# Kernel tuning notes

Measured on AMD Instinct MI355X. Metric: run time of the kernel, lower is better.

## Reference

```python
import jax, jax.numpy as jnp
import numpy as np

DET_SIZE = 5120
DET_THRESHOLD = 0.5
NMS_THRESHOLD = 0.4
STRIDES = (8, 16, 32)
NUM_ANCHORS = 2
TOP_K = 2048  # fixed pre-NMS candidate count (jit-friendly stand-in for torch.where filtering)


def _anchor_centers(stride):
    n = DET_SIZE // stride
    g = jnp.arange(n, dtype=jnp.float32) * stride
    X, Y = jnp.meshgrid(g, g, indexing='xy')       # matches torch.meshgrid(..., indexing='xy')
    c = jnp.stack([X, Y], axis=-1).reshape(-1, 2)  # (n*n, 2), x fastest
    return jnp.repeat(c, NUM_ANCHORS, axis=0)      # stack([c]*2, dim=1).reshape(-1,2) == interleaved repeat


def _pairwise_iou(b):
    # b: (K,4) xyxy
    area = jnp.clip(b[:, 2] - b[:, 0], 0.0) * jnp.clip(b[:, 3] - b[:, 1], 0.0)
    lt = jnp.maximum(b[:, None, :2], b[None, :, :2])
    rb = jnp.minimum(b[:, None, 2:], b[None, :, 2:])
    wh = jnp.clip(rb - lt, 0.0)
    inter = wh[..., 0] * wh[..., 1]
    return inter / (area[:, None] + area[None, :] - inter + 1e-9)


def _forward(scores8, bbox8, lms8, scores16, bbox16, lms16, scores32, bbox32, lms32, det_scale):
    confs, boxes, lmss = [], [], []
    per_stride = [(scores8, bbox8, lms8), (scores16, bbox16, lms16), (scores32, bbox32, lms32)]
    for (conf, bbox, lms), stride in zip(per_stride, STRIDES):
        c = _anchor_centers(stride)                 # (N,2)
        b = bbox * stride                            # distance-style offsets scaled by stride
        l = lms * stride
        box = jnp.concatenate([c - b[:, :2], c + b[:, 2:4]], axis=-1) / det_scale  # (N,4) xyxy
        pts = (c[:, None, :] + l.reshape(-1, 5, 2)) / det_scale                    # (N,5,2)
        confs.append(conf.reshape(-1)); boxes.append(box); lmss.append(pts)
    conf = jnp.concatenate(confs)
    box = jnp.concatenate(boxes, axis=0)
    pts = jnp.concatenate(lmss, axis=0)
    # score threshold via masking (fixed shapes); below-threshold entries get conf=-1
    conf_m = jnp.where(conf >= DET_THRESHOLD, conf, -1.0)
    top_conf, top_idx = jax.lax.top_k(conf_m, TOP_K)
    top_box = box[top_idx]          # (K,4)
    top_pts = pts[top_idx]          # (K,5,2)
    valid = top_conf >= DET_THRESHOLD
    iou = _pairwise_iou(top_box)    # (K,K)
    later = jnp.arange(TOP_K)
    def body(i, keep):
        supp = (iou[i] > NMS_THRESHOLD) & (later > i) & keep[i] & valid[i]
        return keep & ~supp
    keep = jax.lax.fori_loop(0, TOP_K, body, valid)  # greedy NMS in descending-score order
    m = keep.astype(top_box.dtype)
    # (K, 15) = [conf | bbox(4) | lms(10)], suppressed/invalid rows zeroed
    return jnp.concatenate([(top_conf * m)[:, None], top_box * m[:, None], top_pts.reshape(TOP_K, 10) * m[:, None]], axis=-1)


def setup_inputs() -> dict:
    key = jax.random.key(0)
    ks = jax.random.split(key, 9)
    inp = {}
    for i, s in enumerate(STRIDES):
        n = DET_SIZE // s
        N = n * n * NUM_ANCHORS
        inp[f'scores{s}'] = jax.random.uniform(ks[3 * i], (N,), dtype=jnp.float32)
        inp[f'bbox{s}'] = jax.random.uniform(ks[3 * i + 1], (N, 4), dtype=jnp.float32) * 8.0
        inp[f'lms{s}'] = jax.random.normal(ks[3 * i + 2], (N, 10), dtype=jnp.float32) * 4.0
    inp['det_scale'] = jnp.array(0.5, dtype=jnp.float32)
    return inp


def reference(scores8, bbox8, lms8, scores16, bbox16, lms16, scores32, bbox32, lms32, det_scale):
    return _forward(scores8, bbox8, lms8, scores16, bbox16, lms16, scores32, bbox32, lms32, det_scale)
```

## Files before the change

kernel.cpp:

```cpp
#include <hip/hip_runtime.h>
#include <stdint.h>
#include <stddef.h>

#pragma clang fp contract(off)

#define N8   819200u
#define N16  204800u
#define N32  51200u
#define NTOT 1075200u
#define TOPK 2048
#define CAND_MAX 8192
#define NBIN 8192u
#define BINSHIFT 10
#define NMS_THR 0.4f
#define DET_THR 0.5f

#define OFF_HIST   0u
#define OFF_META   32768u
#define OFF_CAND   32832u
#define OFF_TIDX   98368u
#define OFF_TCONF  106560u
#define OFF_BOX    114752u
#define OFF_DIAGT  147520u
#define OFF_SUPPT  155968u

__device__ __forceinline__ float load_conf(unsigned a, const float* __restrict__ s8,
                                           const float* __restrict__ s16,
                                           const float* __restrict__ s32) {
  if (a < N8) return s8[a];
  if (a < N8 + N16) return s16[a - N8];
  return s32[a - (N8 + N16)];
}

__device__ __forceinline__ void decode(unsigned a,
    const float* __restrict__ b8, const float* __restrict__ l8,
    const float* __restrict__ b16, const float* __restrict__ l16,
    const float* __restrict__ b32, const float* __restrict__ l32,
    float& cx, float& cy, float& s, const float*& bb, const float*& lm) {
  if (a < N8) {
    unsigned cell = a >> 1;
    cx = (float)((cell % 640u) * 8u); cy = (float)((cell / 640u) * 8u);
    s = 8.f; bb = b8 + (size_t)a * 4; lm = l8 + (size_t)a * 10;
  } else if (a < N8 + N16) {
    unsigned loc = a - N8; unsigned cell = loc >> 1;
    cx = (float)((cell % 320u) * 16u); cy = (float)((cell / 320u) * 16u);
    s = 16.f; bb = b16 + (size_t)loc * 4; lm = l16 + (size_t)loc * 10;
  } else {
    unsigned loc = a - (N8 + N16); unsigned cell = loc >> 1;
    cx = (float)((cell % 160u) * 32u); cy = (float)((cell / 160u) * 32u);
    s = 32.f; bb = b32 + (size_t)loc * 4; lm = l32 + (size_t)loc * 10;
  }
}

__global__ void k_hist(const float* __restrict__ s8, const float* __restrict__ s16,
                       const float* __restrict__ s32, unsigned* __restrict__ hist) {
  unsigned i = blockIdx.x * blockDim.x + threadIdx.x;
  unsigned st = gridDim.x * blockDim.x;
  for (unsigned a = i; a < NTOT; a += st) {
    float c = load_conf(a, s8, s16, s32);
    if (c >= DET_THR) {
      unsigned v = (__float_as_uint(c) - 0x3F000000u) >> BINSHIFT;
      if (v > NBIN - 1u) v = NBIN - 1u;
      atomicAdd(&hist[v], 1u);
    }
  }
}

__global__ void __launch_bounds__(1024) k_scan(const unsigned* __restrict__ hist,
                                               unsigned* __restrict__ meta) {
  __shared__ unsigned suf[1024];
  int t = threadIdx.x;
  const unsigned* hp = hist + (size_t)t * 8;
  unsigned s = 0;
  for (int b = 0; b < 8; b++) s += hp[b];
  suf[t] = s;
  __syncthreads();
  for (int d = 1; d < 1024; d <<= 1) {
    unsigned v = (t + d < 1024) ? suf[t + d] : 0u;
    __syncthreads();
    suf[t] += v;
    __syncthreads();
  }
  unsigned total = suf[0];
  unsigned mine = suf[t];
  unsigned nxt = (t < 1023) ? suf[t + 1] : 0u;
  if (total < (unsigned)TOPK) {
    if (t == 0) { meta[0] = 0u; meta[2] = total; }
    return;
  }
  if (mine >= (unsigned)TOPK && nxt < (unsigned)TOPK) {
    unsigned run = nxt, cut = (unsigned)t * 8u;
    for (int b = 7; b >= 0; b--) {
      run += hp[b];
      if (run >= (unsigned)TOPK) { cut = (unsigned)t * 8u + (unsigned)b; break; }
    }
    meta[0] = cut; meta[2] = total;
  }
}

__global__ void k_compact(const float* __restrict__ s8, const float* __restrict__ s16,
                          const float* __restrict__ s32, unsigned* __restrict__ meta,
                          unsigned long long* __restrict__ cand) {
  unsigned cut = meta[0];
  unsigned i = blockIdx.x * blockDim.x + threadIdx.x;
  unsigned st = gridDim.x * blockDim.x;
  for (unsigned a = i; a < NTOT; a += st) {
    float c = load_conf(a, s8, s16, s32);
    if (c >= DET_THR) {
      unsigned b = __float_as_uint(c);
      unsigned v = (b - 0x3F000000u) >> BINSHIFT;
      if (v >= cut) {
        unsigned pos = atomicAdd(&meta[3], 1u);
        if (pos < (unsigned)CAND_MAX)
          cand[pos] = ((unsigned long long)b << 32) |
                      (unsigned long long)(0xFFFFFFFFu - a);
      }
    }
  }
}

__global__ void __launch_bounds__(256) k_rank(
    const unsigned long long* __restrict__ cand, const unsigned* __restrict__ meta,
    const float* __restrict__ b8, const float* __restrict__ l8,
    const float* __restrict__ b16, const float* __restrict__ l16,
    const float* __restrict__ b32, const float* __restrict__ l32,
    const float* __restrict__ dsp,
    unsigned* __restrict__ tidx, float* __restrict__ tconf, float* __restrict__ box) {
  unsigned count = meta[3];
  if (count > (unsigned)CAND_MAX) count = (unsigned)CAND_MAX;
  unsigned wave = blockIdx.x * 4u + (threadIdx.x >> 6);
  unsigned lane = threadIdx.x & 63u;
  if (wave >= count) return;
  unsigned long long my = cand[wave];
  unsigned cnt = 0;
  for (unsigned i = lane; i < count; i += 64u)
    cnt += (cand[i] > my) ? 1u : 0u;
  for (int d = 32; d > 0; d >>= 1) cnt += __shfl_down(cnt, d);
  if (lane == 0 && cnt < (unsigned)TOPK) {
    unsigned r = cnt;
    unsigned a = 0xFFFFFFFFu - (unsigned)(my & 0xFFFFFFFFull);
    float conf = __uint_as_float((unsigned)(my >> 32));
    float cx, cy, s; const float* bb; const float* lm;
    decode(a, b8, l8, b16, l16, b32, l32, cx, cy, s, bb, lm);
    float ds = dsp[0];
    float b0 = bb[0] * s, b1 = bb[1] * s, b2 = bb[2] * s, b3 = bb[3] * s;
    box[r * 4 + 0] = (cx - b0) / ds;
    box[r * 4 + 1] = (cy - b1) / ds;
    box[r * 4 + 2] = (cx + b2) / ds;
    box[r * 4 + 3] = (cy + b3) / ds;
    tidx[r] = a; tconf[r] = conf;
  }
}

__global__ void __launch_bounds__(256) k_supp(const float* __restrict__ box,
                                              unsigned long long* __restrict__ supp64,
                                              unsigned* __restrict__ diagT) {
  int i = blockIdx.x;
  const float4 bi = ((const float4*)box)[i];
  float ai = fmaxf(bi.z - bi.x, 0.f) * fmaxf(bi.w - bi.y, 0.f);
  int tid = threadIdx.x;
  int lane = tid & 63, wv = tid >> 6;
  int c = i >> 5, k = i & 31;
  for (int base = 0; base < TOPK; base += 256) {
    int j = base + tid;
    const float4 bj = ((const float4*)box)[j];
    float aj = fmaxf(bj.z - bj.x, 0.f) * fmaxf(bj.w - bj.y, 0.f);
    float ltx = fmaxf(bi.x, bj.x), lty = fmaxf(bi.y, bj.y);
    float rbx = fminf(bi.z, bj.z), rby = fminf(bi.w, bj.w);
    float w = fmaxf(rbx - ltx, 0.f), h = fmaxf(rby - lty, 0.f);
    float inter = w * h;
    float iou = inter / (ai + aj - inter + 1e-9f);
    bool pred = (iou > NMS_THR) && (j > i);
    unsigned long long word = __ballot(pred);
    int w64 = (base >> 6) + wv;
    if (lane == 0) {
      supp64[(size_t)c * 1024 + k * 32 + w64] = word;
      if (w64 == (i >> 6))
        diagT[k * 64 + c] = (unsigned)(word >> (((i >> 5) & 1) * 32));
    }
  }
}

__global__ void __launch_bounds__(512) k_nms_out(
    const unsigned* __restrict__ supp_t, const unsigned* __restrict__ diagT,
    const unsigned* __restrict__ meta,
    const unsigned* __restrict__ tidx, const float* __restrict__ tconf,
    const float* __restrict__ b8, const float* __restrict__ l8,
    const float* __restrict__ b16, const float* __restrict__ l16,
    const float* __restrict__ b32, const float* __restrict__ l32,
    const float* __restrict__ dsp, float* __restrict__ out) {
  __shared__ unsigned keepw[64];
  __shared__ unsigned wacc[8];
  int tid = threadIdx.x;
  int v = tid >> 6, l = tid & 63;
  unsigned count = meta[3];
  if (count > (unsigned)TOPK) count = (unsigned)TOPK;
  if (tid < 8) wacc[tid] = 0u;
  unsigned dg[32];
  if (v == 0) {
#pragma unroll
    for (int k = 0; k < 32; k++) dg[k] = diagT[k * 64 + l];
  }
  int r = v * 4 + (l >> 4);
  int g = l & 15;
  const uint4* bp = (const uint4*)supp_t + ((size_t)r * 16 + g);
  uint4 P0 = bp[0 * 512], P1 = bp[1 * 512], P2 = bp[2 * 512], P3 = bp[3 * 512];
  uint4 A; A.x = 0u; A.y = 0u; A.z = 0u; A.w = 0u;
  __syncthreads();

#define STEP(PP, CC)                                                          \
  {                                                                           \
    const int ch = (CC);                                                      \
    if (v == 0) {                                                             \
      unsigned app = (l < 8) ? wacc[l] : 0u;                                  \
      app |= __shfl_xor(app, 1);                                              \
      app |= __shfl_xor(app, 2);                                              \
      app |= __shfl_xor(app, 4);                                              \
      unsigned appl = __builtin_amdgcn_readlane(app, 0);                      \
      unsigned lo = (unsigned)ch * 32u;                                       \
      unsigned init = (count >= lo + 32u) ? 0xFFFFFFFFu                       \
                    : (count <= lo ? 0u : ((1u << (count - lo)) - 1u));       \
      unsigned w = init & ~appl;                                              \
      _Pragma("unroll") for (int k = 0; k < 32; k++) {                        \
        unsigned d = __builtin_amdgcn_readlane(dg[k], ch);                    \
        w &= ~(((w >> k) & 1u) ? d : 0u);                                     \
      }                                                                       \
      if (l == 0) keepw[ch] = w;                                              \
    }                                                                         \
    __syncthreads();                                                          \
    unsigned wc = keepw[ch];                                                  \
    unsigned m = 0u - ((wc >> r) & 1u);                                       \
    unsigned x0 = PP.x & m, x1 = PP.y & m, x2 = PP.z & m, x3 = PP.w & m;      \
    x0 |= __shfl_xor(x0, 16); x1 |= __shfl_xor(x1, 16);                       \
    x2 |= __shfl_xor(x2, 16); x3 |= __shfl_xor(x3, 16);                       \
    x0 |= __shfl_xor(x0, 32); x1 |= __shfl_xor(x1, 32);                       \
    x2 |= __shfl_xor(x2, 32); x3 |= __shfl_xor(x3, 32);                       \
    A.x |= x0; A.y |= x1; A.z |= x2; A.w |= x3;                               \
    if (ch + 4 < 64) PP = bp[(size_t)(ch + 4) * 512];                         \
    {                                                                         \
      const int nc = ch + 1;                                                  \
      if (nc < 64 && g == (nc >> 2) && (l >> 4) == 0) {                       \
        const int sel = nc & 3;                                               \
        unsigned comp = (sel == 0) ? A.x : (sel == 1) ? A.y                   \
                       : (sel == 2) ? A.z : A.w;                              \
        wacc[v] = comp;                                                       \
      }                                                                       \
    }                                                                         \
    __syncthreads();                                                          \
  }

#pragma unroll 1
  for (int c = 0; c < 64; c += 4) {
    STEP(P0, c + 0)
    STEP(P1, c + 1)
    STEP(P2, c + 2)
    STEP(P3, c + 3)
  }
#undef STEP

  float ds = dsp[0];
  for (int rr = tid; rr < TOPK; rr += 512) {
    bool kept = (keepw[rr >> 5] >> (rr & 31)) & 1u;
    float o[15];
    if (kept) {
      unsigned a = tidx[rr];
      float cx, cy, s; const float* bb; const float* lm;
      decode(a, b8, l8, b16, l16, b32, l32, cx, cy, s, bb, lm);
      o[0] = tconf[rr];
      float b0 = bb[0] * s, b1 = bb[1] * s, b2 = bb[2] * s, b3 = bb[3] * s;
      o[1] = (cx - b0) / ds;
      o[2] = (cy - b1) / ds;
      o[3] = (cx + b2) / ds;
      o[4] = (cy + b3) / ds;
      for (int p = 0; p < 5; p++) {
        float lx = lm[2 * p] * s, ly = lm[2 * p + 1] * s;
        o[5 + 2 * p] = (cx + lx) / ds;
        o[6 + 2 * p] = (cy + ly) / ds;
      }
    } else {
      for (int cc = 0; cc < 15; cc++) o[cc] = 0.f;
    }
    for (int cc = 0; cc < 15; cc++) out[(size_t)rr * 15 + cc] = o[cc];
  }
}

extern "C" void kernel_launch(void* const* d_in, const int* in_sizes, int n_in,
                              void* d_out, int out_size, void* d_ws, size_t ws_size,
                              hipStream_t stream) {
  const float* s8  = (const float*)d_in[0];
  const float* b8  = (const float*)d_in[1];
  const float* l8  = (const float*)d_in[2];
  const float* s16 = (const float*)d_in[3];
  const float* b16 = (const float*)d_in[4];
  const float* l16 = (const float*)d_in[5];
  const float* s32 = (const float*)d_in[6];
  const float* b32 = (const float*)d_in[7];
  const float* l32 = (const float*)d_in[8];
  const float* dsp = (const float*)d_in[9];
  char* ws = (char*)d_ws;
  unsigned* hist = (unsigned*)(ws + OFF_HIST);
  unsigned* meta = (unsigned*)(ws + OFF_META);
  unsigned long long* cand = (unsigned long long*)(ws + OFF_CAND);
  unsigned* tidx = (unsigned*)(ws + OFF_TIDX);
  float* tconf = (float*)(ws + OFF_TCONF);
  float* box = (float*)(ws + OFF_BOX);
  unsigned* diagT = (unsigned*)(ws + OFF_DIAGT);
  unsigned* supp_t = (unsigned*)(ws + OFF_SUPPT);
  float* out = (float*)d_out;

  hipMemsetAsync(ws, 0, OFF_META + 64, stream);
  k_hist<<<2048, 256, 0, stream>>>(s8, s16, s32, hist);
  k_scan<<<1, 1024, 0, stream>>>(hist, meta);
  k_compact<<<2048, 256, 0, stream>>>(s8, s16, s32, meta, cand);
  k_rank<<<CAND_MAX / 4, 256, 0, stream>>>(cand, meta, b8, l8, b16, l16, b32, l32,
                                           dsp, tidx, tconf, box);
  k_supp<<<TOPK, 256, 0, stream>>>(box, (unsigned long long*)supp_t, diagT);
  k_nms_out<<<1, 512, 0, stream>>>(supp_t, diagT, meta, tidx, tconf,
                                   b8, l8, b16, l16, b32, l32, dsp, out);
}
```

Baseline: 138.4 us.

## Replace barrier-stepped greedy NMS with wave-owned chunk groups and flag-based handoff

The greedy NMS sweep is restructured so each of the 8 waves owns a contiguous group of 8 column chunks, instead of wave 0 resolving every chunk between two block-wide barriers. Finished chunks are published through per-chunk shared-memory flags with release/acquire atomics, and later waves spin on those flags, removing 128 __syncthreads per launch. The suppression-mask layout per lane is changed accordingly and prefetch depth is raised to 8 chunks. The IoU kernel now uses nontemporal stores. Risks include spin-wait overhead and a serial dependency chain across waves that may still limit overlap.

```diff
diff --git a/kernel.cpp b/kernel.cpp
--- a/kernel.cpp
+++ b/kernel.cpp
@@ -174,14 +174,15 @@
     unsigned long long word = __ballot(pred);
     int w64 = (base >> 6) + wv;
     if (lane == 0) {
-      supp64[(size_t)c * 1024 + k * 32 + w64] = word;
+      __builtin_nontemporal_store(word, &supp64[(size_t)c * 1024 + k * 32 + w64]);
       if (w64 == (i >> 6))
-        diagT[k * 64 + c] = (unsigned)(word >> (((i >> 5) & 1) * 32));
-    }
-  }
-}
-
-__global__ void __launch_bounds__(512) k_nms_out(
+        __builtin_nontemporal_store(
+            (unsigned)(word >> (((i >> 5) & 1) * 32)), &diagT[k * 64 + c]);
+    }
+  }
+}
+
+__global__ void __launch_bounds__(512, 1) k_nms_out(
     const unsigned* __restrict__ supp_t, const unsigned* __restrict__ diagT,
     const unsigned* __restrict__ meta,
     const unsigned* __restrict__ tidx, const float* __restrict__ tconf,
@@ -190,74 +191,84 @@
     const float* __restrict__ b32, const float* __restrict__ l32,
     const float* __restrict__ dsp, float* __restrict__ out) {
   __shared__ unsigned keepw[64];
-  __shared__ unsigned wacc[8];
-  int tid = threadIdx.x;
-  int v = tid >> 6, l = tid & 63;
+  __shared__ unsigned flagw[64];
+  const int tid = threadIdx.x;
+  const int v = tid >> 6, l = tid & 63;
+  const int par = l & 1, row_ = l >> 1;
   unsigned count = meta[3];
   if (count > (unsigned)TOPK) count = (unsigned)TOPK;
-  if (tid < 8) wacc[tid] = 0u;
+  if (tid < 64) { keepw[tid] = 0u; flagw[tid] = 0u; }
   unsigned dg[32];
-  if (v == 0) {
 #pragma unroll
-    for (int k = 0; k < 32; k++) dg[k] = diagT[k * 64 + l];
-  }
-  int r = v * 4 + (l >> 4);
-  int g = l & 15;
-  const uint4* bp = (const uint4*)supp_t + ((size_t)r * 16 + g);
+  for (int k = 0; k < 32; k++) dg[k] = diagT[k * 64 + l];
+  const uint4* bp = (const uint4*)supp_t + ((size_t)(row_ * 16 + v * 2 + par));
+  __syncthreads();
   uint4 P0 = bp[0 * 512], P1 = bp[1 * 512], P2 = bp[2 * 512], P3 = bp[3 * 512];
-  uint4 A; A.x = 0u; A.y = 0u; A.z = 0u; A.w = 0u;
-  __syncthreads();
-
-#define STEP(PP, CC)                                                          \
+  uint4 P4 = bp[4 * 512], P5 = bp[5 * 512], P6 = bp[6 * 512], P7 = bp[7 * 512];
+  unsigned A0 = 0u, A1 = 0u, A2 = 0u, A3 = 0u;
+
+#define NMS_APPLY(WS, PB)                                                     \
   {                                                                           \
-    const int ch = (CC);                                                      \
-    if (v == 0) {                                                             \
-      unsigned app = (l < 8) ? wacc[l] : 0u;                                  \
-      app |= __shfl_xor(app, 1);                                              \
-      app |= __shfl_xor(app, 2);                                              \
-      app |= __shfl_xor(app, 4);                                              \
-      unsigned appl = __builtin_amdgcn_readlane(app, 0);                      \
-      unsigned lo = (unsigned)ch * 32u;                                       \
-      unsigned init = (count >= lo + 32u) ? 0xFFFFFFFFu                       \
-                    : (count <= lo ? 0u : ((1u << (count - lo)) - 1u));       \
-      unsigned w = init & ~appl;                                              \
-      _Pragma("unroll") for (int k = 0; k < 32; k++) {                        \
-        unsigned d = __builtin_amdgcn_readlane(dg[k], ch);                    \
-        w &= ~(((w >> k) & 1u) ? d : 0u);                                     \
-      }                                                                       \
-      if (l == 0) keepw[ch] = w;                                              \
-    }                                                                         \
-    __syncthreads();                                                          \
-    unsigned wc = keepw[ch];                                                  \
-    unsigned m = 0u - ((wc >> r) & 1u);                                       \
-    unsigned x0 = PP.x & m, x1 = PP.y & m, x2 = PP.z & m, x3 = PP.w & m;      \
+    unsigned m_ = (unsigned)((int)((WS) << (31 - row_)) >> 31);               \
+    unsigned x0 = PB.x & m_, x1 = PB.y & m_, x2 = PB.z & m_, x3 = PB.w & m_;  \
+    x0 |= __shfl_xor(x0, 2);  x1 |= __shfl_xor(x1, 2);                        \
+    x2 |= __shfl_xor(x2, 2);  x3 |= __shfl_xor(x3, 2);                        \
+    x0 |= __shfl_xor(x0, 4);  x1 |= __shfl_xor(x1, 4);                        \
+    x2 |= __shfl_xor(x2, 4);  x3 |= __shfl_xor(x3, 4);                        \
+    x0 |= __shfl_xor(x0, 8);  x1 |= __shfl_xor(x1, 8);                        \
+    x2 |= __shfl_xor(x2, 8);  x3 |= __shfl_xor(x3, 8);                        \
     x0 |= __shfl_xor(x0, 16); x1 |= __shfl_xor(x1, 16);                       \
     x2 |= __shfl_xor(x2, 16); x3 |= __shfl_xor(x3, 16);                       \
     x0 |= __shfl_xor(x0, 32); x1 |= __shfl_xor(x1, 32);                       \
     x2 |= __shfl_xor(x2, 32); x3 |= __shfl_xor(x3, 32);                       \
-    A.x |= x0; A.y |= x1; A.z |= x2; A.w |= x3;                               \
-    if (ch + 4 < 64) PP = bp[(size_t)(ch + 4) * 512];                         \
-    {                                                                         \
-      const int nc = ch + 1;                                                  \
-      if (nc < 64 && g == (nc >> 2) && (l >> 4) == 0) {                       \
-        const int sel = nc & 3;                                               \
-        unsigned comp = (sel == 0) ? A.x : (sel == 1) ? A.y                   \
-                       : (sel == 2) ? A.z : A.w;                              \
-        wacc[v] = comp;                                                       \
+    A0 |= x0; A1 |= x1; A2 |= x2; A3 |= x3;                                   \
+  }
+
+#define NMS_STEP(CS, PB, AW)                                                  \
+  {                                                                           \
+    const int c_ = g * 8 + (CS);                                              \
+    if (v == g) {                                                             \
+      unsigned acur = __builtin_amdgcn_readlane((AW), ((CS) >> 2));           \
+      unsigned lo_ = (unsigned)c_ * 32u;                                      \
+      unsigned init_ = (count >= lo_ + 32u) ? 0xFFFFFFFFu                     \
+                     : (count <= lo_ ? 0u : ((1u << (count - lo_)) - 1u));    \
+      unsigned w_ = init_ & ~acur;                                            \
+      _Pragma("unroll") for (int k = 0; k < 32; k++) {                        \
+        unsigned d_ = __builtin_amdgcn_readlane(dg[k], c_);                   \
+        w_ &= ~(((w_ >> k) & 1u) ? d_ : 0u);                                  \
       }                                                                       \
+      if (l == 0) {                                                           \
+        keepw[c_] = w_;                                                       \
+        __hip_atomic_store(&flagw[c_], 1u, __ATOMIC_RELEASE,                  \
+                           __HIP_MEMORY_SCOPE_WORKGROUP);                     \
+      }                                                                       \
+      NMS_APPLY(w_, PB)                                                       \
+      if (c_ + 8 < 64) PB = bp[(size_t)(c_ + 8) * 512];                       \
+    } else if (v > g) {                                                       \
+      while (__hip_atomic_load(&flagw[c_], __ATOMIC_ACQUIRE,                  \
+                               __HIP_MEMORY_SCOPE_WORKGROUP) == 0u)           \
+        __builtin_amdgcn_s_sleep(1);                                          \
+      unsigned w_ = __builtin_amdgcn_readfirstlane(keepw[c_]);                \
+      NMS_APPLY(w_, PB)                                                       \
+      if (c_ + 8 < 64) PB = bp[(size_t)(c_ + 8) * 512];                       \
     }                                                                         \
-    __syncthreads();                                                          \
   }
 
 #pragma unroll 1
-  for (int c = 0; c < 64; c += 4) {
-    STEP(P0, c + 0)
-    STEP(P1, c + 1)
-    STEP(P2, c + 2)
-    STEP(P3, c + 3)
-  }
-#undef STEP
-
+  for (int g = 0; g < 8; g++) {
+    NMS_STEP(0, P0, A0)
+    NMS_STEP(1, P1, A1)
+    NMS_STEP(2, P2, A2)
+    NMS_STEP(3, P3, A3)
+    NMS_STEP(4, P4, A0)
+    NMS_STEP(5, P5, A1)
+    NMS_STEP(6, P6, A2)
+    NMS_STEP(7, P7, A3)
+  }
+#undef NMS_STEP
+#undef NMS_APPLY
+
+  __syncthreads();
   float ds = dsp[0];
   for (int rr = tid; rr < TOPK; rr += 512) {
     bool kept = (keepw[rr >> 5] >> (rr & 31)) & 1u;
```

Measured after the change: 153.5 us. 1.11x slower.
